# Optimization experiments

Measured on AMD Instinct MI355X. Metric: run time of the kernel, lower is better.

## Reference

```python
import jax, jax.numpy as jnp
import numpy as np

# static module config (init_kwargs)
SLEN = 300       # image side length
PT = 20          # ptile_slen
STEP = 4         # tile stride
EP = 2           # edge_padding
MAXD = 2         # max_detections
NB = 2           # n_bands
NS = 30          # max_sources per full image
NGAL = 8         # n_galaxy_params
B = 8            # batch
N1 = (SLEN - PT) // STEP + 1      # tiles per side (71)
NP_TILES = N1 * N1               # 5041
SUB = B * NP_TILES               # subimage batch


def _ptile_coords():
    # row-major tile corner coords, matches _get_ptile_coords
    i = np.arange(NP_TILES)
    return jnp.asarray(np.stack([i // N1 * STEP, i % N1 * STEP], axis=1), dtype=jnp.float32)


def _tile_images(images):
    # images: [B, C, H, W] -> [B*NP_TILES, C, PT, PT], tiles row-major (x, then y)
    starts = jnp.arange(N1) * STEP
    rows = starts[:, None] + jnp.arange(PT)[None, :]          # [N1, PT]
    p = images[:, :, rows, :]                                  # [B, C, N1, PT, W]
    p = p[:, :, :, :, rows]                                    # [B, C, N1, PT, N1, PT]
    p = jnp.transpose(p, (0, 2, 4, 1, 3, 5))                   # [B, nx, ny, C, PT, PT]
    return p.reshape(SUB, images.shape[1], PT, PT)


def setup_inputs() -> dict:
    key = jax.random.key(0)
    k1, k2, k3, k4 = jax.random.split(key, 4)
    return {
        "images": jax.random.normal(k1, (B, NB, SLEN, SLEN), dtype=jnp.float32),
        "locs": jax.random.uniform(k2, (B, NS, 2), dtype=jnp.float32),
        "galaxy_params": jax.random.normal(k3, (B, NS, NGAL), dtype=jnp.float32),
        "log_fluxes": jax.random.normal(k4, (B, NS, NB), dtype=jnp.float32),
    }


def reference(images, locs, galaxy_params, log_fluxes):
    tc = _ptile_coords()                                       # [NP, 2]
    image_ptiles = _tile_images(images)                        # [SUB, NB, PT, PT]

    # --- _get_params_in_tiles ---
    lp = locs * (SLEN - 1)                                     # pixel coords [B, NS, 2]
    tcb = tc[None, :, None, :]                                 # [1, NP, 1, 2]
    lo = tcb + EP - 0.5
    hi = tcb - 0.5 + PT - EP
    cond = (lp[:, None] > lo) & (lp[:, None] < hi) & (lp[:, None] != 0.0)  # [B, NP, NS, 2]
    which = (cond[..., 0] & cond[..., 1]).astype(images.dtype)             # [B, NP, NS]

    scale = PT - 2 * EP
    tile_locs = (which[..., None] * lp[:, None] - lo).reshape(SUB, NS, 2) / scale
    tile_locs = jax.nn.relu(tile_locs)
    tile_gal = (which[..., None] * galaxy_params[:, None]).reshape(SUB, NS, NGAL)
    tile_flux = (which[..., None] * log_fluxes[:, None]).reshape(SUB, NS, NB)

    is_on = which.reshape(SUB, NS)                             # float {0,1}
    n_src = jnp.sum(is_on, axis=1).astype(jnp.int32)           # [SUB]

    # --- _bring_to_front: stable compaction of 'on' sources to the front ---
    order = jnp.argsort(1.0 - is_on, axis=1, stable=True)      # on-indices first, original order
    mask = (jnp.arange(NS)[None, :] < n_src[:, None]).astype(images.dtype)  # is_on_array_full

    def compact(x):
        return jnp.take_along_axis(x, order[:, :, None], axis=1) * mask[:, :, None]

    # --- _apply_padding_and_clipping: clip to MAXD (NS >= MAXD, no padding needed) ---
    tile_locs = compact(tile_locs)[:, :MAXD]
    tile_gal = compact(tile_gal)[:, :MAXD]
    tile_flux = compact(tile_flux)[:, :MAXD]
    tile_is_on = mask[:, :MAXD].astype(jnp.int32)
    tile_n_sources = jnp.minimum(n_src, MAXD)

    return image_ptiles, tile_locs, tile_gal, tile_flux, tile_n_sources, tile_is_on
```

## Files before the change

kernel.cpp:

```cpp
#include <hip/hip_runtime.h>

#define SLEN   300
#define PT     20
#define STEP   4
#define MAXD   2
#define NBANDS 2
#define NS     30
#define NGAL   8
#define BATCH  8
#define N1     71
#define NPT    (N1*N1)
#define NSUB   (BATCH*NPT)

#define OFF_LOCS 32262400
#define OFF_GAL  32423712
#define OFF_FLUX 33068960
#define OFF_N    33230272
#define OFF_ISON 33270600

#define TILE_BLOCKS (BATCH * N1)
#define CAT_BLOCKS  ((NSUB + 255) / 256)
#define CHUNK (TILE_BLOCKS / 8)

typedef float vf4 __attribute__((ext_vector_type(4)));

__global__ __launch_bounds__(256) void fused_kernel(
    const float* __restrict__ img,
    const float* __restrict__ locs,
    const float* __restrict__ gal,
    const float* __restrict__ flux,
    float* __restrict__ out)
{
    const int bid = blockIdx.x;
    const int tid = threadIdx.x;

    if (bid < TILE_BLOCKS) {
        const int wg = (bid & 7) * CHUNK + (bid >> 3);
        const int i  = wg % N1;
        const int b  = wg / N1;

        const int sub0 = b * NPT + i * N1;
        vf4* dst = reinterpret_cast<vf4*>(out) + (size_t)sub0 * 200;
        const float* imb = img + (size_t)b * NBANDS * SLEN * SLEN
                               + (size_t)(i * STEP) * SLEN;
        const int tot = N1 * 200;
        for (int w = tid; w < tot; w += 256) {
            int jj  = w / 200;
            int rem = w - jj * 200;
            int c   = rem / 100;
            int r2  = rem - c * 100;
            int rr  = r2 / 5;
            int q   = r2 - rr * 5;
            const vf4 v = *reinterpret_cast<const vf4*>(
                imb + ((size_t)(c * SLEN + rr)) * SLEN + jj * 4 + q * 4);
            dst[w] = v;
        }
    } else {
        const int sub = (bid - TILE_BLOCKS) * 256 + tid;
        if (sub >= NSUB) return;

        const int b = sub / NPT;
        const int t = sub % NPT;
        const int i = t / N1;
        const int j = t % N1;

        const float lox = (float)(i * STEP) + 1.5f;
        const float loy = (float)(j * STEP) + 1.5f;
        const float hix = lox + 16.0f;
        const float hiy = loy + 16.0f;

        int   cnt = 0;
        int   sid[2] = {0, 0};
        float slx[2] = {0.f, 0.f};
        float sly[2] = {0.f, 0.f};

        const float* lb = locs + (size_t)b * NS * 2;
        #pragma unroll
        for (int s = 0; s < NS; ++s) {
            float lx = lb[2 * s + 0] * (float)(SLEN - 1);
            float ly = lb[2 * s + 1] * (float)(SLEN - 1);
            bool on = (lx > lox) && (lx < hix) && (ly > loy) && (ly < hiy);
            if (on) {
                if (cnt < MAXD) { sid[cnt] = s; slx[cnt] = lx; sly[cnt] = ly; }
                cnt++;
            }
        }

        const float inv_scale = 1.0f / 16.0f;

        float4 lv;
        lv.x = (cnt > 0) ? fmaxf((slx[0] - lox) * inv_scale, 0.0f) : 0.0f;
        lv.y = (cnt > 0) ? fmaxf((sly[0] - loy) * inv_scale, 0.0f) : 0.0f;
        lv.z = (cnt > 1) ? fmaxf((slx[1] - lox) * inv_scale, 0.0f) : 0.0f;
        lv.w = (cnt > 1) ? fmaxf((sly[1] - loy) * inv_scale, 0.0f) : 0.0f;
        reinterpret_cast<float4*>(out + OFF_LOCS)[sub] = lv;

        float4 g0 = {0,0,0,0}, g1 = {0,0,0,0}, g2 = {0,0,0,0}, g3 = {0,0,0,0};
        if (cnt > 0) {
            const float4* gp = reinterpret_cast<const float4*>(
                gal + ((size_t)(b * NS + sid[0])) * NGAL);
            g0 = gp[0]; g1 = gp[1];
        }
        if (cnt > 1) {
            const float4* gp = reinterpret_cast<const float4*>(
                gal + ((size_t)(b * NS + sid[1])) * NGAL);
            g2 = gp[0]; g3 = gp[1];
        }
        float4* go = reinterpret_cast<float4*>(out + OFF_GAL) + (size_t)sub * 4;
        go[0] = g0; go[1] = g1; go[2] = g2; go[3] = g3;

        float4 fv = {0,0,0,0};
        if (cnt > 0) {
            const float2 f = reinterpret_cast<const float2*>(
                flux + ((size_t)(b * NS + sid[0])) * NBANDS)[0];
            fv.x = f.x; fv.y = f.y;
        }
        if (cnt > 1) {
            const float2 f = reinterpret_cast<const float2*>(
                flux + ((size_t)(b * NS + sid[1])) * NBANDS)[0];
            fv.z = f.x; fv.w = f.y;
        }
        reinterpret_cast<float4*>(out + OFF_FLUX)[sub] = fv;

        out[OFF_N + sub] = (float)(cnt < MAXD ? cnt : MAXD);
        float2 ison;
        ison.x = (cnt > 0) ? 1.0f : 0.0f;
        ison.y = (cnt > 1) ? 1.0f : 0.0f;
        reinterpret_cast<float2*>(out + OFF_ISON)[sub] = ison;
    }
}

extern "C" void kernel_launch(void* const* d_in, const int* in_sizes, int n_in,
                              void* d_out, int out_size, void* d_ws, size_t ws_size,
                              hipStream_t stream)
{
    const float* images = (const float*)d_in[0];
    const float* locs   = (const float*)d_in[1];
    const float* gal    = (const float*)d_in[2];
    const float* flux   = (const float*)d_in[3];
    float* out = (float*)d_out;

    fused_kernel<<<TILE_BLOCKS + CAT_BLOCKS, 256, 0, stream>>>(
        images, locs, gal, flux, out);
}
```

Baseline: 30.51 us.

## Grid-stride tiling copy per batch with XCD-pinned blocks

Replaces the per-row tile copy blocks (one block per batch and tile row) with a grid-stride loop where 236 blocks per batch image stride across that image's whole patch output, and each batch is mapped to one XCD via bid&7. The goal is to spread the memory-bound copy over more blocks and keep each image's source rows in a single XCD's L2 for reuse across overlapping tiles. It adds more index arithmetic per element, and each thread's strided accesses are less local.

```diff
diff --git a/kernel.cpp b/kernel.cpp
--- a/kernel.cpp
+++ b/kernel.cpp
@@ -18,9 +18,11 @@
 #define OFF_N    33230272
 #define OFF_ISON 33270600
 
-#define TILE_BLOCKS (BATCH * N1)
+#define TPX   236
+#define TILE_BLOCKS (8 * TPX)
 #define CAT_BLOCKS  ((NSUB + 255) / 256)
-#define CHUNK (TILE_BLOCKS / 8)
+#define PB    (NPT * 200)
+#define XTHREADS (TPX * 256)
 
 typedef float vf4 __attribute__((ext_vector_type(4)));
 
@@ -35,25 +37,25 @@
     const int tid = threadIdx.x;
 
     if (bid < TILE_BLOCKS) {
-        const int wg = (bid & 7) * CHUNK + (bid >> 3);
-        const int i  = wg % N1;
-        const int b  = wg / N1;
+        const int xcd = bid & 7;
+        const int b   = xcd;
+        const int gt  = (bid >> 3) * 256 + tid;
+        const float* imb = img + (size_t)b * NBANDS * SLEN * SLEN;
+        vf4* dstb = reinterpret_cast<vf4*>(out) + (size_t)b * PB;
 
-        const int sub0 = b * NPT + i * N1;
-        vf4* dst = reinterpret_cast<vf4*>(out) + (size_t)sub0 * 200;
-        const float* imb = img + (size_t)b * NBANDS * SLEN * SLEN
-                               + (size_t)(i * STEP) * SLEN;
-        const int tot = N1 * 200;
-        for (int w = tid; w < tot; w += 256) {
-            int jj  = w / 200;
-            int rem = w - jj * 200;
+        for (int w = gt; w < PB; w += XTHREADS) {
+            int sub = w / 200;
+            int rem = w - sub * 200;
+            int i   = sub / N1;
+            int j   = sub - i * N1;
             int c   = rem / 100;
             int r2  = rem - c * 100;
             int rr  = r2 / 5;
             int q   = r2 - rr * 5;
             const vf4 v = *reinterpret_cast<const vf4*>(
-                imb + ((size_t)(c * SLEN + rr)) * SLEN + jj * 4 + q * 4);
-            dst[w] = v;
+                imb + (size_t)(c * SLEN + i * STEP + rr) * SLEN
+                    + j * STEP + q * 4);
+            dstb[w] = v;
         }
     } else {
         const int sub = (bid - TILE_BLOCKS) * 256 + tid;
```

Result: faster. 28.18 us (-7.7%).
